# Performance work log

Measured on AMD Instinct MI355X. Metric: run time of the kernel, lower is better.

## Reference

```python
import jax, jax.numpy as jnp
import numpy as np

N, K, CONV_DIM = 100, 20, 256
TEMP, ALPHA = 0.1, 0.1
B_NORM = 1  # module hardcodes self.B = 1
BATCH = 8


def setup_inputs() -> dict:
    key = jax.random.key(0)
    inputs = jax.random.normal(key, (BATCH, N, K, CONV_DIM), dtype=jnp.float32)
    return {"inputs": inputs}


def reference(inputs) -> jnp.ndarray:
    # inputs: [B, N, K, D] prototype representations
    B, n, k, D = inputs.shape
    # L2-normalize along feature dim (reduce_euclidean_norm)
    xn = inputs / jnp.sqrt(jnp.sum(inputs * inputs, axis=-1, keepdims=True))
    flat = xn.reshape(B, n * k, D)  # all prototypes, all classes: [B, N*K, D]

    # anchor-vs-all similarities: [B, N, K, N*K]
    sims = jnp.einsum('bnkd,bmd->bnkm', xn, flat) / TEMP
    # anchor self-similarity (==1/t after normalization, but keep exact math): [B, N, K]
    self_sim = jnp.sum(xn * xn, axis=-1) / TEMP

    # denominator: sum_m exp(sim) - exp(self)
    denom = jnp.sum(jnp.exp(sims), axis=-1) - jnp.exp(self_sim)
    log_term = jnp.log(denom)  # [B, N, K]

    # intra-class similarity sum: anchor vs all K prototypes of its own class
    intra = jnp.einsum('bnkd,bnjd->bnk', xn, xn) / TEMP  # [B, N, K]
    sum_term = (intra - self_sim) / (k - 1)

    cl_loss = jnp.sum(log_term - sum_term)  # summed over batch and all N*K anchors
    loss = ALPHA * cl_loss / (B_NORM * n * k * D)
    return loss
```

## Files before the change

### kernel.cpp

```cpp
#include <hip/hip_runtime.h>
#include <math.h>

#define BB 8
#define NN 100
#define KK 20
#define DD 256
#define MM 2000
#define MP 2048
#define TINV 10.0f
#define LOSS_SCALE 1.953125e-7f

typedef __bf16 bf16x8 __attribute__((ext_vector_type(8)));
typedef float floatx4 __attribute__((ext_vector_type(4)));
typedef __attribute__((address_space(1))) const ushort GUshort;
typedef __attribute__((address_space(3))) ushort LUshort;

__device__ __forceinline__ ushort f2bf(float f) {
    unsigned int u = __float_as_uint(f);
    u += 0x7fffu + ((u >> 16) & 1u);
    return (ushort)(u >> 16);
}

__global__ void norm_bf16(const float* __restrict__ x, ushort* __restrict__ xb,
                          float* __restrict__ accbuf, float* __restrict__ out) {
    if (blockIdx.x < 32)
        ((float4*)accbuf)[blockIdx.x * 256 + threadIdx.x] = make_float4(0.f, 0.f, 0.f, 0.f);
    if (blockIdx.x == 0 && threadIdx.x == 0) out[0] = 0.0f;

    const int rg = blockIdx.x * 4 + (threadIdx.x >> 6);
    const int lane = threadIdx.x & 63;
    const int b = rg >> 11;
    const int r = rg & (MP - 1);
    ushort4 outv = make_ushort4(0, 0, 0, 0);
    if (r < MM) {
        const float4 v = ((const float4*)(x + ((size_t)(b * MM + r)) * DD))[lane];
        float s = v.x * v.x + v.y * v.y + v.z * v.z + v.w * v.w;
        #pragma unroll
        for (int o = 32; o >= 1; o >>= 1) s += __shfl_xor(s, o, 64);
        const float inv = 1.0f / sqrtf(s);
        outv.x = f2bf(v.x * inv);
        outv.y = f2bf(v.y * inv);
        outv.z = f2bf(v.z * inv);
        outv.w = f2bf(v.w * inv);
    }
    ((ushort4*)(xb + (size_t)rg * DD))[lane] = outv;
}

__global__ __launch_bounds__(256)
void cl_mfma(const ushort* __restrict__ xb,
             float* __restrict__ denom_g, float* __restrict__ intra_g) {
    __shared__ __align__(16) ushort As[128 * 64];
    __shared__ __align__(16) ushort Bs[128 * 64];

    const int b = blockIdx.x & 7;
    const int ti = (blockIdx.x >> 3) & 15;
    const int tj = blockIdx.x >> 7;
    const int rbase = ti << 7;
    const int cbase = tj << 7;
    const ushort* __restrict__ xbb = xb + (size_t)b * MP * DD;

    const int tid = threadIdx.x;
    const int lane = tid & 63;
    const int w = tid >> 6;
    const int wr = (w >> 1) << 6;
    const int wc = (w & 1) << 6;
    const int tx = lane & 15;
    const int tx7 = tx & 7;
    const int quad = lane >> 4;

    const int srow = lane >> 3;
    const int sg = (lane & 7) ^ srow;

    floatx4 acc[4][4];
    #pragma unroll
    for (int mt = 0; mt < 4; ++mt)
        #pragma unroll
        for (int nt = 0; nt < 4; ++nt)
            acc[mt][nt] = (floatx4){0.f, 0.f, 0.f, 0.f};

    #pragma unroll 1
    for (int kc = 0; kc < 4; ++kc) {
        __syncthreads();
        #pragma unroll
        for (int q = 0; q < 4; ++q) {
            const int R = ((w << 2) + q) << 3;
            const size_t koff = (kc << 6) + (sg << 3);
            __builtin_amdgcn_global_load_lds(
                (GUshort*)(xbb + (size_t)(rbase + R + srow) * DD + koff),
                (LUshort*)(As + R * 64), 16, 0, 0);
            __builtin_amdgcn_global_load_lds(
                (GUshort*)(xbb + (size_t)(cbase + R + srow) * DD + koff),
                (LUshort*)(Bs + R * 64), 16, 0, 0);
        }
        __syncthreads();

        #pragma unroll
        for (int ks = 0; ks < 2; ++ks) {
            const int g = (ks << 2) + quad;
            const int gp = (g ^ tx7) << 3;
            bf16x8 af[4], bf[4];
            #pragma unroll
            for (int mt = 0; mt < 4; ++mt)
                af[mt] = *(const bf16x8*)(As + (wr + (mt << 4) + tx) * 64 + gp);
            #pragma unroll
            for (int nt = 0; nt < 4; ++nt)
                bf[nt] = *(const bf16x8*)(Bs + (wc + (nt << 4) + tx) * 64 + gp);
            #pragma unroll
            for (int mt = 0; mt < 4; ++mt)
                #pragma unroll
                for (int nt = 0; nt < 4; ++nt)
                    acc[mt][nt] = __builtin_amdgcn_mfma_f32_16x16x32_bf16(af[mt], bf[nt], acc[mt][nt], 0, 0, 0);
        }
    }

    int colv[4], colcls[4];
    bool colok[4];
    #pragma unroll
    for (int nt = 0; nt < 4; ++nt) {
        const int c = cbase + wc + (nt << 4) + tx;
        colv[nt] = c;
        colok[nt] = c < MM;
        colcls[nt] = c / KK;
    }

    #pragma unroll
    for (int mt = 0; mt < 4; ++mt) {
        #pragma unroll
        for (int i = 0; i < 4; ++i) {
            const int row = rbase + wr + (mt << 4) + (quad << 2) + i;
            const int rcls = row / KK;
            float de = 0.f, it = 0.f;
            #pragma unroll
            for (int nt = 0; nt < 4; ++nt) {
                const float sim = acc[mt][nt][i] * TINV;
                const bool ok = colok[nt] && (colv[nt] != row);
                de += ok ? __expf(sim) : 0.0f;
                it += (ok && (colcls[nt] == rcls)) ? sim : 0.0f;
            }
            #pragma unroll
            for (int o = 8; o >= 1; o >>= 1) {
                de += __shfl_xor(de, o, 64);
                it += __shfl_xor(it, o, 64);
            }
            if (tx == 0) {
                atomicAdd(&denom_g[b * MP + row], de);
                atomicAdd(&intra_g[b * MP + row], it);
            }
        }
    }
}

__global__ void finalize_kernel(const float* __restrict__ denom_g,
                                const float* __restrict__ intra_g,
                                float* __restrict__ out) {
    const int i = blockIdx.x * 256 + threadIdx.x;
    float s = 0.0f;
    if (i < BB * MM) {
        const int b = i / MM;
        const int r = i - b * MM;
        s = logf(denom_g[b * MP + r]) - intra_g[b * MP + r] * (1.0f / (KK - 1));
    }
    #pragma unroll
    for (int o = 32; o >= 1; o >>= 1) s += __shfl_xor(s, o, 64);
    __shared__ float red[4];
    if ((threadIdx.x & 63) == 0) red[threadIdx.x >> 6] = s;
    __syncthreads();
    if (threadIdx.x == 0)
        atomicAdd(out, (red[0] + red[1] + red[2] + red[3]) * LOSS_SCALE);
}

extern "C" void kernel_launch(void* const* d_in, const int* in_sizes, int n_in,
                              void* d_out, int out_size, void* d_ws, size_t ws_size,
                              hipStream_t stream) {
    const float* x = (const float*)d_in[0];
    float* out = (float*)d_out;
    float* denom_g = (float*)d_ws;
    float* intra_g = denom_g + BB * MP;
    ushort* xb = (ushort*)(intra_g + BB * MP);

    norm_bf16<<<BB * MP / 4, 256, 0, stream>>>(x, xb, denom_g, out);
    cl_mfma<<<BB * 16 * 16, 256, 0, stream>>>(xb, denom_g, intra_g);
    finalize_kernel<<<(BB * MM + 255) / 256, 256, 0, stream>>>(denom_g, intra_g, out);
}
```

Baseline: 105.8 us.

## Compute intra-class term via class-sum norm identity instead of in GEMM epilogue

The intra-class similarity sum is rewritten algebraically as the squared norm of each class's summed normalized vectors minus K, and is computed in fp32 in the finalize kernel from the raw inputs and stored inverse norms. This removes the class comparison, the second shuffle reduction and the second atomic from the MFMA epilogue, and drops the intra buffer. In exchange the finalize kernel rereads the fp32 input (about 16 MB) across 800 extra blocks, and the norm kernel now also writes inverse norms.

```diff
diff --git a/kernel.cpp b/kernel.cpp
--- a/kernel.cpp
+++ b/kernel.cpp
@@ -22,9 +22,10 @@
 }
 
 __global__ void norm_bf16(const float* __restrict__ x, ushort* __restrict__ xb,
-                          float* __restrict__ accbuf, float* __restrict__ out) {
-    if (blockIdx.x < 32)
-        ((float4*)accbuf)[blockIdx.x * 256 + threadIdx.x] = make_float4(0.f, 0.f, 0.f, 0.f);
+                          float* __restrict__ invn_out,
+                          float* __restrict__ denom_g, float* __restrict__ out) {
+    if (blockIdx.x < 16)
+        ((float4*)denom_g)[blockIdx.x * 256 + threadIdx.x] = make_float4(0.f, 0.f, 0.f, 0.f);
     if (blockIdx.x == 0 && threadIdx.x == 0) out[0] = 0.0f;
 
     const int rg = blockIdx.x * 4 + (threadIdx.x >> 6);
@@ -38,6 +39,7 @@
         #pragma unroll
         for (int o = 32; o >= 1; o >>= 1) s += __shfl_xor(s, o, 64);
         const float inv = 1.0f / sqrtf(s);
+        if (lane == 0) invn_out[rg] = inv;
         outv.x = f2bf(v.x * inv);
         outv.y = f2bf(v.y * inv);
         outv.z = f2bf(v.z * inv);
@@ -47,8 +49,7 @@
 }
 
 __global__ __launch_bounds__(256)
-void cl_mfma(const ushort* __restrict__ xb,
-             float* __restrict__ denom_g, float* __restrict__ intra_g) {
+void cl_mfma(const ushort* __restrict__ xb, float* __restrict__ denom_g) {
     __shared__ __align__(16) ushort As[128 * 64];
     __shared__ __align__(16) ushort Bs[128 * 64];
 
@@ -113,14 +114,13 @@
         }
     }
 
-    int colv[4], colcls[4];
+    int colv[4];
     bool colok[4];
     #pragma unroll
     for (int nt = 0; nt < 4; ++nt) {
         const int c = cbase + wc + (nt << 4) + tx;
         colv[nt] = c;
         colok[nt] = c < MM;
-        colcls[nt] = c / KK;
     }
 
     #pragma unroll
@@ -128,45 +128,62 @@
         #pragma unroll
         for (int i = 0; i < 4; ++i) {
             const int row = rbase + wr + (mt << 4) + (quad << 2) + i;
-            const int rcls = row / KK;
-            float de = 0.f, it = 0.f;
+            float de = 0.f;
             #pragma unroll
             for (int nt = 0; nt < 4; ++nt) {
-                const float sim = acc[mt][nt][i] * TINV;
-                const bool ok = colok[nt] && (colv[nt] != row);
-                de += ok ? __expf(sim) : 0.0f;
-                it += (ok && (colcls[nt] == rcls)) ? sim : 0.0f;
+                const float e = __expf(acc[mt][nt][i] * TINV);
+                de += (colok[nt] && (colv[nt] != row)) ? e : 0.0f;
             }
             #pragma unroll
-            for (int o = 8; o >= 1; o >>= 1) {
+            for (int o = 8; o >= 1; o >>= 1)
                 de += __shfl_xor(de, o, 64);
-                it += __shfl_xor(it, o, 64);
-            }
-            if (tx == 0) {
+            if (tx == 0)
                 atomicAdd(&denom_g[b * MP + row], de);
-                atomicAdd(&intra_g[b * MP + row], it);
-            }
-        }
-    }
-}
-
-__global__ void finalize_kernel(const float* __restrict__ denom_g,
-                                const float* __restrict__ intra_g,
-                                float* __restrict__ out) {
-    const int i = blockIdx.x * 256 + threadIdx.x;
-    float s = 0.0f;
-    if (i < BB * MM) {
-        const int b = i / MM;
-        const int r = i - b * MM;
-        s = logf(denom_g[b * MP + r]) - intra_g[b * MP + r] * (1.0f / (KK - 1));
-    }
-    #pragma unroll
-    for (int o = 32; o >= 1; o >>= 1) s += __shfl_xor(s, o, 64);
+        }
+    }
+}
+
+__global__ void finalize_combined(const float* __restrict__ x,
+                                  const float* __restrict__ invn,
+                                  const float* __restrict__ denom_g,
+                                  float* __restrict__ out) {
     __shared__ float red[4];
-    if ((threadIdx.x & 63) == 0) red[threadIdx.x >> 6] = s;
-    __syncthreads();
-    if (threadIdx.x == 0)
-        atomicAdd(out, (red[0] + red[1] + red[2] + red[3]) * LOSS_SCALE);
+    const int tid = threadIdx.x;
+    if (blockIdx.x < 800) {
+        const int g = blockIdx.x;
+        const int b = g / NN;
+        const int n = g - b * NN;
+        const int row0 = n * KK;
+        const float* __restrict__ xg = x + ((size_t)(b * MM + row0)) * DD;
+        const float* __restrict__ ig = invn + b * MP + row0;
+        float s = 0.0f;
+        #pragma unroll
+        for (int k = 0; k < KK; ++k)
+            s = fmaf(ig[k], xg[(size_t)k * DD + tid], s);
+        float v = s * s;
+        #pragma unroll
+        for (int o = 32; o >= 1; o >>= 1) v += __shfl_xor(v, o, 64);
+        if ((tid & 63) == 0) red[tid >> 6] = v;
+        __syncthreads();
+        if (tid == 0) {
+            const float S2 = red[0] + red[1] + red[2] + red[3];
+            atomicAdd(out, -LOSS_SCALE * (TINV / (KK - 1)) * (S2 - (float)KK));
+        }
+    } else {
+        const int i = (blockIdx.x - 800) * 256 + tid;
+        float s = 0.0f;
+        if (i < BB * MM) {
+            const int b = i / MM;
+            const int r = i - b * MM;
+            s = logf(denom_g[b * MP + r]);
+        }
+        #pragma unroll
+        for (int o = 32; o >= 1; o >>= 1) s += __shfl_xor(s, o, 64);
+        if ((tid & 63) == 0) red[tid >> 6] = s;
+        __syncthreads();
+        if (tid == 0)
+            atomicAdd(out, (red[0] + red[1] + red[2] + red[3]) * LOSS_SCALE);
+    }
 }
 
 extern "C" void kernel_launch(void* const* d_in, const int* in_sizes, int n_in,
@@ -175,10 +192,10 @@
     const float* x = (const float*)d_in[0];
     float* out = (float*)d_out;
     float* denom_g = (float*)d_ws;
-    float* intra_g = denom_g + BB * MP;
-    ushort* xb = (ushort*)(intra_g + BB * MP);
-
-    norm_bf16<<<BB * MP / 4, 256, 0, stream>>>(x, xb, denom_g, out);
-    cl_mfma<<<BB * 16 * 16, 256, 0, stream>>>(xb, denom_g, intra_g);
-    finalize_kernel<<<(BB * MM + 255) / 256, 256, 0, stream>>>(denom_g, intra_g, out);
-}
+    float* invn = denom_g + BB * MP;
+    ushort* xb = (ushort*)(invn + BB * MP);
+
+    norm_bf16<<<BB * MP / 4, 256, 0, stream>>>(x, xb, invn, denom_g, out);
+    cl_mfma<<<BB * 16 * 16, 256, 0, stream>>>(xb, denom_g);
+    finalize_combined<<<800 + 63, 256, 0, stream>>>(x, invn, denom_g, out);
+}
```

Result: slower. 114.1 us (+7.8%).
